# Optimization experiments

Measured on AMD Instinct MI355X. Metric: run time of the kernel, lower is better.

The kernel has to match this reference:

```python
import jax, jax.numpy as jnp
import numpy as np

B, N, M, D = 8, 4096, 4096, 2


def setup_inputs() -> dict:
    key = jax.random.key(0)
    k1, k2 = jax.random.split(key)
    x = jax.random.normal(k1, (B, N, D), dtype=jnp.float32)
    target = jax.random.normal(k2, (B, M, D), dtype=jnp.float32)
    return {"x": x, "target": target}


def reference(x, target):
    # Pairwise squared Euclidean distances [B, N, M] via the expansion
    # ||a-b||^2 = ||a||^2 + ||b||^2 - 2 a.b  (matmul-friendly form).
    x2 = jnp.sum(x * x, axis=-1)            # [B, N]
    t2 = jnp.sum(target * target, axis=-1)  # [B, M]
    cross = jnp.einsum("bnd,bmd->bnm", x, target)  # [B, N, M]
    d2 = x2[:, :, None] + t2[:, None, :] - 2.0 * cross
    d2 = jnp.maximum(d2, 0.0)  # numerical floor before sqrt
    # tree1.query(array2[i]): for each target point, distance to nearest x point.
    d_t_to_x = jnp.sqrt(jnp.min(d2, axis=1))  # [B, M]
    # tree2.query(array1[i]): for each x point, distance to nearest target point.
    d_x_to_t = jnp.sqrt(jnp.min(d2, axis=2))  # [B, N]
    # sum over batch of (mean1 + mean2)/B == mean of per-batch means (equal sizes).
    return jnp.mean(d_t_to_x) + jnp.mean(d_x_to_t)
```

## Files before the change

kernel.cpp:

```cpp
#include <hip/hip_runtime.h>
#include <math.h>

#define NPTS  4096
#define BQ    64
#define RQ    16
#define SLOTS 4
#define NS    128
#define CHUNK 32
#define CF4   16
#define PCF4  17

__global__ __launch_bounds__(512, 6) void chamfer_main(
    const float* __restrict__ x, const float* __restrict__ tgt,
    float* __restrict__ partials)
{
    __shared__ float4 sm[NS * PCF4];
    __shared__ float  red[8 * BQ];

    const int bx  = blockIdx.x;
    const int dir = bx >> 9;
    const int b   = (bx >> 6) & 7;
    const int qt  = bx & 63;
    const int t   = threadIdx.x;
    const int lane = t & 63, w = t >> 6;

    const float* qarr = dir ? tgt : x;
    const float* sarr = dir ? x   : tgt;

    const float4* sp4 = (const float4*)(sarr + b * (NPTS * 2));
    #pragma unroll
    for (int k = 0; k < 4; ++k) {
        const int i = t + k * 512;
        sm[i + (i >> 4)] = sp4[i];
    }

    const int slot = t & (SLOTS - 1);
    const int s    = t >> 2;
    const float2* qp = (const float2*)(qarr + b * (NPTS * 2));
    float nx[RQ], ny[RQ], m[RQ];
    #pragma unroll
    for (int r = 0; r < RQ; ++r) {
        const float2 p = qp[qt * BQ + slot + SLOTS * r];
        nx[r] = -2.f * p.x;
        ny[r] = -2.f * p.y;
        m[r]  = INFINITY;
    }
    __syncthreads();

    const float4* tp = sm + s * PCF4;
    #pragma unroll 4
    for (int j = 0; j < CF4; ++j) {
        const float4 t4 = tp[j];
        const float z0 = fmaf(t4.x, t4.x, t4.y * t4.y);
        const float z1 = fmaf(t4.z, t4.z, t4.w * t4.w);
        #pragma unroll
        for (int r = 0; r < RQ; ++r) {
            const float d0 = fmaf(nx[r], t4.x, fmaf(ny[r], t4.y, z0));
            const float d1 = fmaf(nx[r], t4.z, fmaf(ny[r], t4.w, z1));
            m[r] = fminf(fminf(m[r], d0), d1);
        }
    }

    #pragma unroll
    for (int r = 0; r < RQ; ++r)
        m[r] += 0.25f * fmaf(nx[r], nx[r], ny[r] * ny[r]);

    #pragma unroll
    for (int r = 0; r < RQ; ++r) {
        m[r] = fminf(m[r], __shfl_xor(m[r], 4));
        m[r] = fminf(m[r], __shfl_xor(m[r], 8));
        m[r] = fminf(m[r], __shfl_xor(m[r], 16));
        m[r] = fminf(m[r], __shfl_xor(m[r], 32));
    }
    if (lane < SLOTS) {
        #pragma unroll
        for (int r = 0; r < RQ; ++r) red[w * BQ + lane + SLOTS * r] = m[r];
    }
    __syncthreads();

    if (t < BQ) {
        float mm = red[t];
        #pragma unroll
        for (int ww = 1; ww < 8; ++ww) mm = fminf(mm, red[ww * BQ + t]);
        float v = sqrtf(fmaxf(mm, 0.f));
        v += __shfl_down(v, 32);
        v += __shfl_down(v, 16);
        v += __shfl_down(v, 8);
        v += __shfl_down(v, 4);
        v += __shfl_down(v, 2);
        v += __shfl_down(v, 1);
        if (t == 0) partials[bx] = v;
    }
}

__global__ __launch_bounds__(256) void chamfer_final(
    const float* __restrict__ partials, float* __restrict__ out)
{
    __shared__ float red[256];
    const int tid = threadIdx.x;
    float v = partials[tid] + partials[tid + 256] +
              partials[tid + 512] + partials[tid + 768];
    red[tid] = v;
    __syncthreads();
    if (tid < 64) {
        float s = red[tid] + red[tid + 64] + red[tid + 128] + red[tid + 192];
        s += __shfl_down(s, 32);
        s += __shfl_down(s, 16);
        s += __shfl_down(s, 8);
        s += __shfl_down(s, 4);
        s += __shfl_down(s, 2);
        s += __shfl_down(s, 1);
        if (tid == 0) out[0] = s * (1.0f / 32768.0f);
    }
}

extern "C" void kernel_launch(void* const* d_in, const int* in_sizes, int n_in,
                              void* d_out, int out_size, void* d_ws, size_t ws_size,
                              hipStream_t stream) {
    const float* x   = (const float*)d_in[0];
    const float* tgt = (const float*)d_in[1];
    float* partials  = (float*)d_ws;
    float* out       = (float*)d_out;

    chamfer_main<<<dim3(1024), dim3(512), 0, stream>>>(x, tgt, partials);
    chamfer_final<<<dim3(1),   dim3(256), 0, stream>>>(partials, out);
}
```

Before: 26.24 us.

## Compute pairwise distances via bf16x3-split MFMA GEMM with atomic min reductions

Replaces the scalar FMA distance loop with a matrix-core formulation. Coordinates and squared norms are split into three bf16 parts packed into the K dimension of mfma 16x16x32 so that one MFMA produces squared distances at near-fp32 accuracy. Both directions' minima come from the same GEMM tile: row minima go to global memory through atomicMin on float bits, and column minima go to shared memory first and then global. This adds a memset and an extra reduction kernel, and relies on int-ordered atomics for non-negative floats, which can break if a slightly negative d2 from rounding appears.

```diff
diff --git a/kernel.cpp b/kernel.cpp
--- a/kernel.cpp
+++ b/kernel.cpp
@@ -1,117 +1,172 @@
 #include <hip/hip_runtime.h>
 #include <math.h>
 
-#define NPTS  4096
-#define BQ    64
-#define RQ    16
-#define SLOTS 4
-#define NS    128
-#define CHUNK 32
-#define CF4   16
-#define PCF4  17
+#define NPTS 4096
 
-__global__ __launch_bounds__(512, 6) void chamfer_main(
+typedef short bf16x8 __attribute__((ext_vector_type(8)));
+typedef float f32x4  __attribute__((ext_vector_type(4)));
+#define INF __builtin_huge_valf()
+
+static __device__ __forceinline__ unsigned short rne16(float v, float* f) {
+    unsigned u = __float_as_uint(v);
+    unsigned r = (u + 0x7FFFu + ((u >> 16) & 1u)) & 0xFFFF0000u;
+    *f = __uint_as_float(r);
+    return (unsigned short)(r >> 16);
+}
+struct S3 { unsigned short h, m, l; };
+static __device__ __forceinline__ S3 split3(float v) {
+    S3 s; float hf, mf, lf;
+    s.h = rne16(v, &hf);
+    float r1 = v - hf;
+    s.m = rne16(r1, &mf);
+    float r2 = r1 - mf;
+    s.l = rne16(r2, &lf);
+    return s;
+}
+
+__global__ __launch_bounds__(512, 2) void chamfer_gemm(
     const float* __restrict__ x, const float* __restrict__ tgt,
-    float* __restrict__ partials)
+    int* __restrict__ gn, int* __restrict__ gm)
 {
-    __shared__ float4 sm[NS * PCF4];
-    __shared__ float  red[8 * BQ];
+    __shared__ short bfrag[64][64][8];
+    __shared__ int   smmin[4096];
 
-    const int bx  = blockIdx.x;
-    const int dir = bx >> 9;
-    const int b   = (bx >> 6) & 7;
-    const int qt  = bx & 63;
+    const int bid = blockIdx.x;
+    const int b   = bid >> 5;
+    const int nc  = (bid >> 2) & 7;
+    const int mq  = bid & 3;
     const int t   = threadIdx.x;
-    const int lane = t & 63, w = t >> 6;
+    const int l   = t & 63, w = t >> 6;
+    const int kw  = l >> 4, row = l & 15;
 
-    const float* qarr = dir ? tgt : x;
-    const float* sarr = dir ? x   : tgt;
+    #pragma unroll
+    for (int k = 0; k < 8; ++k) smmin[t + 512 * k] = 0x7F7F7F7F;
 
-    const float4* sp4 = (const float4*)(sarr + b * (NPTS * 2));
+    const float2* bp = (const float2*)(tgt + b * (NPTS * 2)) + mq * 1024;
     #pragma unroll
-    for (int k = 0; k < 4; ++k) {
-        const int i = t + k * 512;
-        sm[i + (i >> 4)] = sp4[i];
+    for (int k = 0; k < 2; ++k) {
+        const int ml = t + k * 512;
+        const float2 p = bp[ml];
+        const S3 sx = split3(p.x), sy = split3(p.y);
+        const S3 sq = split3(fmaf(p.x, p.x, p.y * p.y));
+        const unsigned H0 = (unsigned)sx.h | ((unsigned)sy.h << 16);
+        const unsigned H1 = 0x3F80u      | ((unsigned)sq.h << 16);
+        const unsigned M0 = (unsigned)sx.m | ((unsigned)sy.m << 16);
+        const unsigned M1 =                 ((unsigned)sq.m << 16);
+        const unsigned L0 = (unsigned)sx.l | ((unsigned)sy.l << 16);
+        const unsigned L1 =                 ((unsigned)sq.l << 16);
+        const int tile = ml >> 4, col = ml & 15;
+        *(uint4*)&bfrag[tile][ 0 + col][0] = make_uint4(H0, H1, M0, M1);
+        *(uint4*)&bfrag[tile][16 + col][0] = make_uint4(L0, L1, H0, H1);
+        *(uint4*)&bfrag[tile][32 + col][0] = make_uint4(M0, M1, H0, H1);
+        *(uint4*)&bfrag[tile][48 + col][0] = make_uint4(0, 0, 0, 0);
     }
 
-    const int slot = t & (SLOTS - 1);
-    const int s    = t >> 2;
-    const float2* qp = (const float2*)(qarr + b * (NPTS * 2));
-    float nx[RQ], ny[RQ], m[RQ];
+    const float2* ap = (const float2*)(x + b * (NPTS * 2));
+    bf16x8 af[4];
     #pragma unroll
-    for (int r = 0; r < RQ; ++r) {
-        const float2 p = qp[qt * BQ + slot + SLOTS * r];
-        nx[r] = -2.f * p.x;
-        ny[r] = -2.f * p.y;
-        m[r]  = INFINITY;
+    for (int tt = 0; tt < 4; ++tt) {
+        const float2 p = ap[nc * 512 + w * 64 + tt * 16 + row];
+        const S3 sx = split3(-2.f * p.x), sy = split3(-2.f * p.y);
+        const S3 sq = split3(fmaf(p.x, p.x, p.y * p.y));
+        const unsigned short e0 = kw < 2 ? sx.h : (kw == 2 ? sx.m : (unsigned short)0);
+        const unsigned short e1 = kw < 2 ? sy.h : (kw == 2 ? sy.m : (unsigned short)0);
+        const unsigned short e2 = kw < 2 ? sq.h : (kw == 2 ? sq.m : (unsigned short)0);
+        const unsigned short e3 = kw < 2 ? (unsigned short)0x3F80 : (unsigned short)0;
+        const unsigned short e4 = kw == 0 ? sx.h : (kw == 1 ? sx.m : (kw == 2 ? sx.l : (unsigned short)0));
+        const unsigned short e5 = kw == 0 ? sy.h : (kw == 1 ? sy.m : (kw == 2 ? sy.l : (unsigned short)0));
+        const unsigned short e6 = kw == 0 ? sq.h : (kw == 1 ? sq.m : (kw == 2 ? sq.l : (unsigned short)0));
+        const unsigned short e7 = kw == 0 ? (unsigned short)0x3F80 : (unsigned short)0;
+        bf16x8 A;
+        A[0] = (short)e0; A[1] = (short)e1; A[2] = (short)e2; A[3] = (short)e3;
+        A[4] = (short)e4; A[5] = (short)e5; A[6] = (short)e6; A[7] = (short)e7;
+        af[tt] = A;
     }
+
     __syncthreads();
 
-    const float4* tp = sm + s * PCF4;
-    #pragma unroll 4
-    for (int j = 0; j < CF4; ++j) {
-        const float4 t4 = tp[j];
-        const float z0 = fmaf(t4.x, t4.x, t4.y * t4.y);
-        const float z1 = fmaf(t4.z, t4.z, t4.w * t4.w);
+    const bf16x8* bptr = (const bf16x8*)&bfrag[0][0][0];
+    const f32x4 zero = {0.f, 0.f, 0.f, 0.f};
+    f32x4 nmin[4];
+    #pragma unroll
+    for (int tt = 0; tt < 4; ++tt) { nmin[tt][0]=INF; nmin[tt][1]=INF; nmin[tt][2]=INF; nmin[tt][3]=INF; }
+
+    #pragma unroll 2
+    for (int mt = 0; mt < 64; mt += 2) {
+        const bf16x8 b0 = bptr[(mt    ) * 64 + l];
+        const bf16x8 b1 = bptr[(mt + 1) * 64 + l];
+        float cm0 = INF, cm1 = INF;
         #pragma unroll
-        for (int r = 0; r < RQ; ++r) {
-            const float d0 = fmaf(nx[r], t4.x, fmaf(ny[r], t4.y, z0));
-            const float d1 = fmaf(nx[r], t4.z, fmaf(ny[r], t4.w, z1));
-            m[r] = fminf(fminf(m[r], d0), d1);
+        for (int tt = 0; tt < 4; ++tt) {
+            const f32x4 c0 = __builtin_amdgcn_mfma_f32_16x16x32_bf16(af[tt], b0, zero, 0, 0, 0);
+            const f32x4 c1 = __builtin_amdgcn_mfma_f32_16x16x32_bf16(af[tt], b1, zero, 0, 0, 0);
+            #pragma unroll
+            for (int r = 0; r < 4; ++r)
+                nmin[tt][r] = fminf(fminf(nmin[tt][r], c0[r]), c1[r]);
+            cm0 = fminf(fminf(fminf(c0[0], c0[1]), fminf(c0[2], c0[3])), cm0);
+            cm1 = fminf(fminf(fminf(c1[0], c1[1]), fminf(c1[2], c1[3])), cm1);
+        }
+        atomicMin(&smmin[kw * 1024 + mt * 16 + row],      __float_as_int(cm0));
+        atomicMin(&smmin[kw * 1024 + mt * 16 + 16 + row], __float_as_int(cm1));
+    }
+
+    #pragma unroll
+    for (int tt = 0; tt < 4; ++tt) {
+        #pragma unroll
+        for (int r = 0; r < 4; ++r) {
+            float v = nmin[tt][r];
+            v = fminf(v, __shfl_xor(v, 1));
+            v = fminf(v, __shfl_xor(v, 2));
+            v = fminf(v, __shfl_xor(v, 4));
+            v = fminf(v, __shfl_xor(v, 8));
+            if (row == 0)
+                atomicMin(&gn[b * 4096 + nc * 512 + w * 64 + tt * 16 + kw * 4 + r],
+                          __float_as_int(v));
         }
     }
 
+    __syncthreads();
     #pragma unroll
-    for (int r = 0; r < RQ; ++r)
-        m[r] += 0.25f * fmaf(nx[r], nx[r], ny[r] * ny[r]);
-
-    #pragma unroll
-    for (int r = 0; r < RQ; ++r) {
-        m[r] = fminf(m[r], __shfl_xor(m[r], 4));
-        m[r] = fminf(m[r], __shfl_xor(m[r], 8));
-        m[r] = fminf(m[r], __shfl_xor(m[r], 16));
-        m[r] = fminf(m[r], __shfl_xor(m[r], 32));
-    }
-    if (lane < SLOTS) {
-        #pragma unroll
-        for (int r = 0; r < RQ; ++r) red[w * BQ + lane + SLOTS * r] = m[r];
-    }
-    __syncthreads();
-
-    if (t < BQ) {
-        float mm = red[t];
-        #pragma unroll
-        for (int ww = 1; ww < 8; ++ww) mm = fminf(mm, red[ww * BQ + t]);
-        float v = sqrtf(fmaxf(mm, 0.f));
-        v += __shfl_down(v, 32);
-        v += __shfl_down(v, 16);
-        v += __shfl_down(v, 8);
-        v += __shfl_down(v, 4);
-        v += __shfl_down(v, 2);
-        v += __shfl_down(v, 1);
-        if (t == 0) partials[bx] = v;
+    for (int k = 0; k < 2; ++k) {
+        const int i = t + k * 512;
+        const int v = min(min(smmin[i], smmin[i + 1024]),
+                          min(smmin[i + 2048], smmin[i + 3072]));
+        atomicMin(&gm[b * 4096 + mq * 1024 + i], v);
     }
 }
 
-__global__ __launch_bounds__(256) void chamfer_final(
-    const float* __restrict__ partials, float* __restrict__ out)
+__global__ __launch_bounds__(256) void chamfer_red1(
+    const int* __restrict__ mins, float* __restrict__ part)
 {
-    __shared__ float red[256];
-    const int tid = threadIdx.x;
-    float v = partials[tid] + partials[tid + 256] +
-              partials[tid + 512] + partials[tid + 768];
-    red[tid] = v;
+    __shared__ float wsum[4];
+    const int t = threadIdx.x;
+    const int4 v = ((const int4*)mins)[blockIdx.x * 256 + t];
+    float s = sqrtf(fmaxf(__int_as_float(v.x), 0.f))
+            + sqrtf(fmaxf(__int_as_float(v.y), 0.f))
+            + sqrtf(fmaxf(__int_as_float(v.z), 0.f))
+            + sqrtf(fmaxf(__int_as_float(v.w), 0.f));
+    s += __shfl_down(s, 32);
+    s += __shfl_down(s, 16);
+    s += __shfl_down(s, 8);
+    s += __shfl_down(s, 4);
+    s += __shfl_down(s, 2);
+    s += __shfl_down(s, 1);
+    if ((t & 63) == 0) wsum[t >> 6] = s;
     __syncthreads();
-    if (tid < 64) {
-        float s = red[tid] + red[tid + 64] + red[tid + 128] + red[tid + 192];
-        s += __shfl_down(s, 32);
-        s += __shfl_down(s, 16);
-        s += __shfl_down(s, 8);
-        s += __shfl_down(s, 4);
-        s += __shfl_down(s, 2);
-        s += __shfl_down(s, 1);
-        if (tid == 0) out[0] = s * (1.0f / 32768.0f);
-    }
+    if (t == 0) part[blockIdx.x] = (wsum[0] + wsum[1]) + (wsum[2] + wsum[3]);
+}
+
+__global__ __launch_bounds__(64) void chamfer_red2(
+    const float* __restrict__ part, float* __restrict__ out)
+{
+    float v = part[threadIdx.x];
+    v += __shfl_down(v, 32);
+    v += __shfl_down(v, 16);
+    v += __shfl_down(v, 8);
+    v += __shfl_down(v, 4);
+    v += __shfl_down(v, 2);
+    v += __shfl_down(v, 1);
+    if (threadIdx.x == 0) out[0] = v * (1.0f / 32768.0f);
 }
 
 extern "C" void kernel_launch(void* const* d_in, const int* in_sizes, int n_in,
@@ -119,9 +174,13 @@
                               hipStream_t stream) {
     const float* x   = (const float*)d_in[0];
     const float* tgt = (const float*)d_in[1];
-    float* partials  = (float*)d_ws;
-    float* out       = (float*)d_out;
+    int*   gn   = (int*)d_ws;
+    int*   gm   = gn + 32768;
+    float* part = (float*)(gn + 65536);
+    float* out  = (float*)d_out;
 
-    chamfer_main<<<dim3(1024), dim3(512), 0, stream>>>(x, tgt, partials);
-    chamfer_final<<<dim3(1),   dim3(256), 0, stream>>>(partials, out);
+    hipMemsetAsync(d_ws, 0x7F, 65536 * sizeof(int), stream);
+    chamfer_gemm<<<dim3(256), dim3(512), 0, stream>>>(x, tgt, gn, gm);
+    chamfer_red1<<<dim3(64),  dim3(256), 0, stream>>>(gn, part);
+    chamfer_red2<<<dim3(1),   dim3(64),  0, stream>>>(part, out);
 }
```

Result: slower. 30.50 us (+16.3%).
